# Optimization experiments

Hardware: AMD Instinct MI355X
Metric: run time of the kernel (lower is better)

Reference implementation:

```python
import jax, jax.numpy as jnp
import numpy as np
from jax import lax

IMAGE_SIZE = 4096.0
IOU_THRESHOLD = 0.5
SCORE_THRESHOLD = 0.05
NUM_CLASSES = 8
TILE = 512
GRID = 8          # 8x8 tiles
N_PER_TILE = 128


def setup_inputs() -> dict:
    key = jax.random.key(0)
    k1, k2, k3, k4, k5 = jax.random.split(key, 5)
    T = GRID * GRID
    N = N_PER_TILE
    # valid boxes in tile-local coords [0, TILE]
    x1 = jax.random.uniform(k1, (T, N, 2), minval=0.0, maxval=TILE - 64.0)  # (x1, y1)
    wh = jax.random.uniform(k2, (T, N, 2), minval=5.0, maxval=64.0)
    x2 = x1 + wh                                                            # (x2, y2)
    boxes = jnp.concatenate([x1, x2], axis=-1)                              # [T,N,4]
    scores = jax.random.uniform(k3, (T, N, 1), minval=0.0, maxval=1.0)
    labels = jax.random.randint(k4, (T, N, 1), 0, NUM_CLASSES).astype(jnp.float32)
    growths = jax.random.normal(k5, (T, N, 1), dtype=jnp.float32)
    tile_results = jnp.concatenate([boxes, scores, labels, growths], axis=-1)  # [T,N,7]

    rows = np.arange(T) // GRID
    cols = np.arange(T) % GRID
    tile_positions = np.stack(
        [rows * TILE, rows * TILE + TILE, cols * TILE, cols * TILE + TILE], axis=1
    ).astype(np.int32)  # (h_start, h_end, w_start, w_end)
    return {"tile_results": tile_results, "tile_positions": jnp.asarray(tile_positions)}


def _pairwise_iou(b):
    # b: [M,4] -> [M,M]
    area = (b[:, 2] - b[:, 0]) * (b[:, 3] - b[:, 1])
    lt = jnp.maximum(b[:, None, :2], b[None, :, :2])
    rb = jnp.minimum(b[:, None, 2:], b[None, :, 2:])
    wh = jnp.clip(rb - lt, 0.0)
    inter = wh[..., 0] * wh[..., 1]
    union = area[:, None] + area[None, :] - inter
    return inter / (union + 1e-8)


def reference(tile_results, tile_positions):
    T, N, _ = tile_results.shape
    M = T * N
    boxes = tile_results[..., :4]        # [T,N,4]
    scores = tile_results[..., 4]        # [T,N]
    labels = tile_results[..., 5].astype(jnp.int32)
    growths = tile_results[..., 6]

    # per-tile offset (x += w_start, y += h_start) and clamp to image
    h_start = tile_positions[:, 0].astype(boxes.dtype)[:, None, None]
    w_start = tile_positions[:, 2].astype(boxes.dtype)[:, None, None]
    offset = jnp.concatenate([w_start, h_start, w_start, h_start], axis=-1)  # [T,1,4]
    boxes = jnp.clip(boxes + offset, 0.0, IMAGE_SIZE)

    boxes = boxes.reshape(M, 4)
    scores = scores.reshape(M)
    labels = labels.reshape(M)
    growths = growths.reshape(M)

    valid = scores > SCORE_THRESHOLD
    # sort by score desc; invalid boxes pushed to the end
    sort_key = scores - 1e9 * (1.0 - valid.astype(scores.dtype))
    order = jnp.argsort(-sort_key)
    boxes_s = boxes[order]
    scores_s = scores[order]
    labels_s = labels[order]
    growths_s = growths[order]
    valid_s = valid[order]

    # per-class NMS == global NMS on class-offset boxes (cross-class IoU = 0)
    class_shift = labels_s.astype(boxes.dtype)[:, None] * (2.0 * IMAGE_SIZE)
    iou = _pairwise_iou(boxes_s + class_shift)  # [M,M], the 268MB working set

    idx = jnp.arange(M)

    def body(i, keep):
        sup = keep[i] & (iou[i] > IOU_THRESHOLD) & (idx > i)
        return keep & ~sup

    keep = lax.fori_loop(0, M, body, valid_s)

    result = jnp.concatenate(
        [boxes_s, scores_s[:, None], labels_s.astype(boxes.dtype)[:, None], growths_s[:, None]],
        axis=1,
    )
    # fixed-shape output: suppressed / filtered rows zeroed, keep mask returned
    return result * keep[:, None].astype(result.dtype), keep
```

## Files before the change

### kernel.cpp

```cpp
#include <hip/hip_runtime.h>

#define NB       128
#define M_TOTAL  8192
#define RESULT_FLOATS (M_TOTAL * 7)

typedef unsigned long long u64;
typedef unsigned int u32;

__global__ __launch_bounds__(512) void fused_nms_kernel(
    const float* __restrict__ tr,
    const int*   __restrict__ tp,
    float*       __restrict__ out)
{
    __shared__ u64   s_boxaug[32];
    __shared__ u64   s_laug[NB];
    __shared__ float t_x1[NB], t_y1[NB], t_x2[NB], t_y2[NB], t_area[NB];
    __shared__ alignas(16) u32 sup32[NB][4];
    __shared__ u64   validmask[2];
    __shared__ u64   keepmask[2];
    __shared__ alignas(16) u32 s_wpart[8][16];
    __shared__ int   s_p[NB];

    const int tid = threadIdx.x;
    const int wv  = tid >> 6;
    const int sub = blockIdx.x & 3;
    const int tb  = blockIdx.x >> 2;
    const int g0  = tb * NB;

    if (tid < 2) validmask[tid] = 0ull;

    float sc[18];
    float sc2[2];
    int   j2 = 0;
    if (wv < 7) {
#pragma unroll
        for (int k = 0; k < 18; ++k)
            sc[k] = tr[(size_t)(tid + 448 * k) * 7 + 4];
    } else {
        j2 = 8064 + ((tid - 448) << 1);
        sc2[0] = tr[(size_t)j2 * 7 + 4];
        sc2[1] = tr[(size_t)(j2 + 1) * 7 + 4];
    }

    if (tid < 32) {
        int i = g0 + sub * 32 + tid;
        float s = tr[(size_t)i * 7 + 4];
        u32 sb = (s > 0.05f) ? __float_as_uint(s) : 0u;
        s_boxaug[tid] = ((u64)sb << 13) | (u64)(M_TOTAL - 1 - i);
    }

    float sx1 = 0.f, sy1 = 0.f, sx2 = 0.f, sy2 = 0.f, area = 0.f;
    u64 aug_n = 0;
    bool valid = false;
    if (tid < NB) {
        const float* row = tr + (size_t)(g0 + tid) * 7;
        float x1 = row[0], y1 = row[1], x2 = row[2], y2 = row[3];
        float score = row[4], label = row[5];
        float hf = (float)tp[tb * 4 + 0];
        float wf = (float)tp[tb * 4 + 2];
        float gx1 = fminf(fmaxf(__fadd_rn(x1, wf), 0.0f), 4096.0f);
        float gy1 = fminf(fmaxf(__fadd_rn(y1, hf), 0.0f), 4096.0f);
        float gx2 = fminf(fmaxf(__fadd_rn(x2, wf), 0.0f), 4096.0f);
        float gy2 = fminf(fmaxf(__fadd_rn(y2, hf), 0.0f), 4096.0f);
        valid = score > 0.05f;
        u32 sb = valid ? __float_as_uint(score) : 0u;
        aug_n = ((u64)sb << 13) | (u64)(M_TOTAL - 1 - (g0 + tid));
        float c = __fmul_rn(label, 8192.0f);
        sx1 = __fadd_rn(gx1, c);
        sy1 = __fadd_rn(gy1, c);
        sx2 = __fadd_rn(gx2, c);
        sy2 = __fadd_rn(gy2, c);
        area = __fmul_rn(__fsub_rn(sx2, sx1), __fsub_rn(sy2, sy1));
        s_laug[tid] = aug_n;
    }
    __syncthreads();

    u64 bk[32];
#pragma unroll
    for (int b = 0; b < 32; ++b) bk[b] = s_boxaug[b];

    if (tid < NB) {
        int p = 0;
        const ulonglong2* lv = (const ulonglong2*)s_laug;
#pragma unroll 8
        for (int u = 0; u < 64; ++u) {
            ulonglong2 v = lv[u];
            p += (v.x > aug_n) + (v.y > aug_n);
        }
        t_x1[p] = sx1; t_y1[p] = sy1; t_x2[p] = sx2; t_y2[p] = sy2;
        t_area[p] = area;
        s_p[tid] = p;
        if (valid) atomicOr(&validmask[p >> 6], 1ull << (p & 63));
    }
    __syncthreads();

    {
        int r = tid >> 2, cq = tid & 3;
        float rx1 = t_x1[r], ry1 = t_y1[r], rx2 = t_x2[r], ry2 = t_y2[r];
        float ra = t_area[r];
        u32 m = 0;
        int wbase = cq * 32;
#pragma unroll 4
        for (int w2 = 0; w2 < 32; ++w2) {
            int w = wbase + w2;
            float ltx = fmaxf(rx1, t_x1[w]);
            float lty = fmaxf(ry1, t_y1[w]);
            float rbx = fminf(rx2, t_x2[w]);
            float rby = fminf(ry2, t_y2[w]);
            float iw = fmaxf(__fsub_rn(rbx, ltx), 0.0f);
            float ih = fmaxf(__fsub_rn(rby, lty), 0.0f);
            float inter = __fmul_rn(iw, ih);
            float uni   = __fsub_rn(__fadd_rn(ra, t_area[w]), inter);
            float denom = __fadd_rn(uni, 1e-8f);
            float iou   = __fdiv_rn(inter, denom);
            bool s = (w > r) && (iou > 0.5f);
            m |= ((u32)s) << w2;
        }
        sup32[r][cq] = m;
    }
    __syncthreads();

    int cnt[32];
#pragma unroll
    for (int b = 0; b < 32; ++b) cnt[b] = 0;

    if (wv < 7) {
#pragma unroll
        for (int k = 0; k < 18; ++k) {
            int j = tid + 448 * k;
            u32 sb = (sc[k] > 0.05f) ? __float_as_uint(sc[k]) : 0u;
            u64 a = ((u64)sb << 13) | (u64)(M_TOTAL - 1 - j);
#pragma unroll
            for (int b = 0; b < 32; ++b) cnt[b] += (a > bk[b]);
        }
    } else {
        if (tid == 448) {
            const ulonglong2* supv = (const ulonglong2*)sup32;
            u64 v0 = validmask[0], v1 = validmask[1];
            u64 r0 = 0ull, r1 = 0ull;
            for (int c = 0; c < NB; c += 8) {
                ulonglong2 buf[8];
#pragma unroll
                for (int x = 0; x < 8; ++x) buf[x] = supv[c + x];
#pragma unroll
                for (int x = 0; x < 8; ++x) {
                    int q = c + x;
                    u64 alive = ((q < 64) ? ((v0 & ~r0) >> q)
                                          : ((v1 & ~r1) >> (q - 64))) & 1ull;
                    u64 take = 0ull - alive;
                    r0 |= buf[x].x & take;
                    r1 |= buf[x].y & take;
                }
            }
            keepmask[0] = v0 & ~r0;
            keepmask[1] = v1 & ~r1;
        }
#pragma unroll
        for (int k = 0; k < 2; ++k) {
            int j = j2 + k;
            float s = sc2[k];
            u32 sb = (s > 0.05f) ? __float_as_uint(s) : 0u;
            u64 a = ((u64)sb << 13) | (u64)(M_TOTAL - 1 - j);
#pragma unroll
            for (int b = 0; b < 32; ++b) cnt[b] += (a > bk[b]);
        }
    }

    u32 pk[16];
#pragma unroll
    for (int q = 0; q < 16; ++q)
        pk[q] = (u32)cnt[q] | ((u32)cnt[q + 16] << 16);

#pragma unroll
    for (int q = 0; q < 16; ++q) {
        int c = (int)pk[q];
#pragma unroll
        for (int m = 1; m < 64; m <<= 1) c += __shfl_xor(c, m, 64);
        pk[q] = (u32)c;
    }
    {
        const int lane = tid & 63;
        if (lane == 0) {
            uint4* wp = (uint4*)&s_wpart[wv][0];
#pragma unroll
            for (int q4 = 0; q4 < 4; ++q4)
                wp[q4] = make_uint4(pk[4*q4], pk[4*q4+1], pk[4*q4+2], pk[4*q4+3]);
        }
    }
    __syncthreads();

    if (tid < 32) {
        int rank = 0;
        const int q = tid & 15;
        const int sh = (tid >> 4) << 4;
#pragma unroll
        for (int w = 0; w < 8; ++w)
            rank += (int)((s_wpart[w][q] >> sh) & 0xffffu);

        int nl = sub * 32 + tid;
        int i  = g0 + nl;
        int pp = s_p[nl];
        float kf = ((keepmask[pp >> 6] >> (pp & 63)) & 1ull) ? 1.0f : 0.0f;

        const float* row = tr + (size_t)i * 7;
        float x1 = row[0], y1 = row[1], x2 = row[2], y2 = row[3];
        float score = row[4], label = row[5], growth = row[6];
        float hf = (float)tp[tb * 4 + 0];
        float wf = (float)tp[tb * 4 + 2];
        float gx1 = fminf(fmaxf(__fadd_rn(x1, wf), 0.0f), 4096.0f);
        float gy1 = fminf(fmaxf(__fadd_rn(y1, hf), 0.0f), 4096.0f);
        float gx2 = fminf(fmaxf(__fadd_rn(x2, wf), 0.0f), 4096.0f);
        float gy2 = fminf(fmaxf(__fadd_rn(y2, hf), 0.0f), 4096.0f);

        float* o = out + (size_t)rank * 7;
        o[0] = __fmul_rn(gx1, kf);
        o[1] = __fmul_rn(gy1, kf);
        o[2] = __fmul_rn(gx2, kf);
        o[3] = __fmul_rn(gy2, kf);
        o[4] = __fmul_rn(score, kf);
        o[5] = __fmul_rn(label, kf);
        o[6] = __fmul_rn(growth, kf);
        out[RESULT_FLOATS + rank] = kf;
    }
}

extern "C" void kernel_launch(void* const* d_in, const int* in_sizes, int n_in,
                              void* d_out, int out_size, void* d_ws, size_t ws_size,
                              hipStream_t stream) {
    const float* tile_results   = (const float*)d_in[0];
    const int*   tile_positions = (const int*)d_in[1];
    float* out = (float*)d_out;

    hipLaunchKernelGGL(fused_nms_kernel, dim3(256), dim3(512), 0, stream,
                       tile_results, tile_positions, out);
}
```

Before: 69.82 us.

## Skip lower-triangle IoU tiles, replace division with threshold compare, cache rows in LDS

```diff
diff --git a/kernel.cpp b/kernel.cpp
--- a/kernel.cpp
+++ b/kernel.cpp
@@ -12,22 +12,20 @@
     const int*   __restrict__ tp,
     float*       __restrict__ out)
 {
-    __shared__ u64   s_boxaug[32];
     __shared__ u64   s_laug[NB];
     __shared__ float t_x1[NB], t_y1[NB], t_x2[NB], t_y2[NB], t_area[NB];
     __shared__ alignas(16) u32 sup32[NB][4];
-    __shared__ u64   validmask[2];
     __shared__ u64   keepmask[2];
     __shared__ alignas(16) u32 s_wpart[8][16];
     __shared__ int   s_p[NB];
+    __shared__ float s_row[7][NB];
+    __shared__ int   s_nv[2];
 
     const int tid = threadIdx.x;
     const int wv  = tid >> 6;
     const int sub = blockIdx.x & 3;
     const int tb  = blockIdx.x >> 2;
     const int g0  = tb * NB;
-
-    if (tid < 2) validmask[tid] = 0ull;
 
     float sc[18];
     float sc2[2];
@@ -42,26 +40,22 @@
         sc2[1] = tr[(size_t)(j2 + 1) * 7 + 4];
     }
 
-    if (tid < 32) {
-        int i = g0 + sub * 32 + tid;
-        float s = tr[(size_t)i * 7 + 4];
-        u32 sb = (s > 0.05f) ? __float_as_uint(s) : 0u;
-        s_boxaug[tid] = ((u64)sb << 13) | (u64)(M_TOTAL - 1 - i);
-    }
-
     float sx1 = 0.f, sy1 = 0.f, sx2 = 0.f, sy2 = 0.f, area = 0.f;
     u64 aug_n = 0;
     bool valid = false;
     if (tid < NB) {
         const float* row = tr + (size_t)(g0 + tid) * 7;
         float x1 = row[0], y1 = row[1], x2 = row[2], y2 = row[3];
-        float score = row[4], label = row[5];
+        float score = row[4], label = row[5], growth = row[6];
         float hf = (float)tp[tb * 4 + 0];
         float wf = (float)tp[tb * 4 + 2];
         float gx1 = fminf(fmaxf(__fadd_rn(x1, wf), 0.0f), 4096.0f);
         float gy1 = fminf(fmaxf(__fadd_rn(y1, hf), 0.0f), 4096.0f);
         float gx2 = fminf(fmaxf(__fadd_rn(x2, wf), 0.0f), 4096.0f);
         float gy2 = fminf(fmaxf(__fadd_rn(y2, hf), 0.0f), 4096.0f);
+        s_row[0][tid] = gx1; s_row[1][tid] = gy1;
+        s_row[2][tid] = gx2; s_row[3][tid] = gy2;
+        s_row[4][tid] = score; s_row[5][tid] = label; s_row[6][tid] = growth;
         valid = score > 0.05f;
         u32 sb = valid ? __float_as_uint(score) : 0u;
         aug_n = ((u64)sb << 13) | (u64)(M_TOTAL - 1 - (g0 + tid));
@@ -72,12 +66,19 @@
         sy2 = __fadd_rn(gy2, c);
         area = __fmul_rn(__fsub_rn(sx2, sx1), __fsub_rn(sy2, sy1));
         s_laug[tid] = aug_n;
+        u64 bm = __ballot(valid);
+        if ((tid & 63) == 0) s_nv[tid >> 6] = (int)__popcll(bm);
     }
     __syncthreads();
 
     u64 bk[32];
 #pragma unroll
-    for (int b = 0; b < 32; ++b) bk[b] = s_boxaug[b];
+    for (int b = 0; b < 32; ++b) {
+        u64 v = s_laug[(sub << 5) + b];
+        u32 lo = (u32)__builtin_amdgcn_readfirstlane((int)(u32)v);
+        u32 hi = (u32)__builtin_amdgcn_readfirstlane((int)(u32)(v >> 32));
+        bk[b] = ((u64)hi << 32) | (u64)lo;
+    }
 
     if (tid < NB) {
         int p = 0;
@@ -90,33 +91,58 @@
         t_x1[p] = sx1; t_y1[p] = sy1; t_x2[p] = sx2; t_y2[p] = sy2;
         t_area[p] = area;
         s_p[tid] = p;
-        if (valid) atomicOr(&validmask[p >> 6], 1ull << (p & 63));
     }
     __syncthreads();
 
     {
-        int r = tid >> 2, cq = tid & 3;
-        float rx1 = t_x1[r], ry1 = t_y1[r], rx2 = t_x2[r], ry2 = t_y2[r];
-        float ra = t_area[r];
-        u32 m = 0;
-        int wbase = cq * 32;
+        const int cq = wv & 3;
+        const int rg = wv >> 2;
+        const int r  = (rg << 6) + (tid & 63);
+        if (rg == 1 && cq < 2) {
+            sup32[r][cq] = 0u;
+        } else {
+            const int wbase = cq * 32;
+            float rx1 = t_x1[r], ry1 = t_y1[r], rx2 = t_x2[r], ry2 = t_y2[r];
+            float ra = t_area[r];
+            u32 m = 0, bnd = 0;
 #pragma unroll 4
-        for (int w2 = 0; w2 < 32; ++w2) {
-            int w = wbase + w2;
-            float ltx = fmaxf(rx1, t_x1[w]);
-            float lty = fmaxf(ry1, t_y1[w]);
-            float rbx = fminf(rx2, t_x2[w]);
-            float rby = fminf(ry2, t_y2[w]);
-            float iw = fmaxf(__fsub_rn(rbx, ltx), 0.0f);
-            float ih = fmaxf(__fsub_rn(rby, lty), 0.0f);
-            float inter = __fmul_rn(iw, ih);
-            float uni   = __fsub_rn(__fadd_rn(ra, t_area[w]), inter);
-            float denom = __fadd_rn(uni, 1e-8f);
-            float iou   = __fdiv_rn(inter, denom);
-            bool s = (w > r) && (iou > 0.5f);
-            m |= ((u32)s) << w2;
-        }
-        sup32[r][cq] = m;
+            for (int w2 = 0; w2 < 32; ++w2) {
+                int w = wbase + w2;
+                float ltx = fmaxf(rx1, t_x1[w]);
+                float lty = fmaxf(ry1, t_y1[w]);
+                float rbx = fminf(rx2, t_x2[w]);
+                float rby = fminf(ry2, t_y2[w]);
+                float iw = fmaxf(__fsub_rn(rbx, ltx), 0.0f);
+                float ih = fmaxf(__fsub_rn(rby, lty), 0.0f);
+                float inter = __fmul_rn(iw, ih);
+                float uni   = __fsub_rn(__fadd_rn(ra, t_area[w]), inter);
+                float denom = __fadd_rn(uni, 1e-8f);
+                float half = __fmul_rn(0.5f, denom);
+                float diff = __fsub_rn(inter, half);
+                bool gt = diff > 0.0f;
+                m   |= ((u32)((w > r) && gt)) << w2;
+                bnd |= ((u32)(fabsf(diff) <= __fmul_rn(denom, 1e-6f))) << w2;
+            }
+            if (__builtin_expect(bnd != 0u, 0)) {
+                for (int w2 = 0; w2 < 32; ++w2) {
+                    if ((bnd >> w2) & 1u) {
+                        int w = wbase + w2;
+                        float ltx = fmaxf(rx1, t_x1[w]);
+                        float lty = fmaxf(ry1, t_y1[w]);
+                        float rbx = fminf(rx2, t_x2[w]);
+                        float rby = fminf(ry2, t_y2[w]);
+                        float iw = fmaxf(__fsub_rn(rbx, ltx), 0.0f);
+                        float ih = fmaxf(__fsub_rn(rby, lty), 0.0f);
+                        float inter = __fmul_rn(iw, ih);
+                        float uni   = __fsub_rn(__fadd_rn(ra, t_area[w]), inter);
+                        float denom = __fadd_rn(uni, 1e-8f);
+                        bool s = (w > r) && (__fdiv_rn(inter, denom) > 0.5f);
+                        m = (m & ~(1u << w2)) | (((u32)s) << w2);
+                    }
+                }
+            }
+            sup32[r][cq] = m;
+        }
     }
     __syncthreads();
 
@@ -135,8 +161,11 @@
         }
     } else {
         if (tid == 448) {
+            int nv = s_nv[0] + s_nv[1];
+            u64 v0 = (nv >= 64) ? ~0ull : ((1ull << nv) - 1ull);
+            u64 v1 = (nv <= 64) ? 0ull
+                   : ((nv >= 128) ? ~0ull : ((1ull << (nv - 64)) - 1ull));
             const ulonglong2* supv = (const ulonglong2*)sup32;
-            u64 v0 = validmask[0], v1 = validmask[1];
             u64 r0 = 0ull, r1 = 0ull;
             for (int c = 0; c < NB; c += 8) {
                 ulonglong2 buf[8];
@@ -197,29 +226,18 @@
         for (int w = 0; w < 8; ++w)
             rank += (int)((s_wpart[w][q] >> sh) & 0xffffu);
 
-        int nl = sub * 32 + tid;
-        int i  = g0 + nl;
+        int nl = (sub << 5) + tid;
         int pp = s_p[nl];
         float kf = ((keepmask[pp >> 6] >> (pp & 63)) & 1ull) ? 1.0f : 0.0f;
 
-        const float* row = tr + (size_t)i * 7;
-        float x1 = row[0], y1 = row[1], x2 = row[2], y2 = row[3];
-        float score = row[4], label = row[5], growth = row[6];
-        float hf = (float)tp[tb * 4 + 0];
-        float wf = (float)tp[tb * 4 + 2];
-        float gx1 = fminf(fmaxf(__fadd_rn(x1, wf), 0.0f), 4096.0f);
-        float gy1 = fminf(fmaxf(__fadd_rn(y1, hf), 0.0f), 4096.0f);
-        float gx2 = fminf(fmaxf(__fadd_rn(x2, wf), 0.0f), 4096.0f);
-        float gy2 = fminf(fmaxf(__fadd_rn(y2, hf), 0.0f), 4096.0f);
-
         float* o = out + (size_t)rank * 7;
-        o[0] = __fmul_rn(gx1, kf);
-        o[1] = __fmul_rn(gy1, kf);
-        o[2] = __fmul_rn(gx2, kf);
-        o[3] = __fmul_rn(gy2, kf);
-        o[4] = __fmul_rn(score, kf);
-        o[5] = __fmul_rn(label, kf);
-        o[6] = __fmul_rn(growth, kf);
+        o[0] = __fmul_rn(s_row[0][nl], kf);
+        o[1] = __fmul_rn(s_row[1][nl], kf);
+        o[2] = __fmul_rn(s_row[2][nl], kf);
+        o[3] = __fmul_rn(s_row[3][nl], kf);
+        o[4] = __fmul_rn(s_row[4][nl], kf);
+        o[5] = __fmul_rn(s_row[5][nl], kf);
+        o[6] = __fmul_rn(s_row[6][nl], kf);
         out[RESULT_FLOATS + rank] = kf;
     }
 }
```

Result: no change. 69.06 us (-1.1%).
